# Kernel tuning notes

Measured on AMD Instinct MI355X. Metric: run time of the kernel, lower is better.

The kernel has to match this reference:

```python
import jax, jax.numpy as jnp
import numpy as np

N_PAPER = 100000
N_AUTHOR = 50000
E = 800000
D_IN, D_HID, D_OUT = 128, 128, 64


def seg_max(x, src, dst, num_segments):
    # adj_t.matmul(x, reduce='max'): per-destination max over neighbor features;
    # destinations with no in-edges get 0 (torch_sparse convention).
    m = jax.ops.segment_max(x[src], dst, num_segments=num_segments)
    return jnp.where(jnp.isneginf(m), jnp.zeros((), m.dtype), m)


def setup_inputs() -> dict:
    key = jax.random.key(0)
    ks = jax.random.split(key, 32)
    inp = {}
    inp['x_paper'] = jax.random.normal(ks[0], (N_PAPER, D_IN), jnp.float32)
    inp['emb_author'] = jax.random.normal(ks[1], (N_AUTHOR, D_IN), jnp.float32)
    inp['writes_src'] = jax.random.randint(ks[2], (E,), 0, N_AUTHOR, jnp.int32)
    inp['writes_dst'] = jax.random.randint(ks[3], (E,), 0, N_PAPER, jnp.int32)
    inp['cites_src'] = jax.random.randint(ks[4], (E,), 0, N_PAPER, jnp.int32)
    inp['cites_dst'] = jax.random.randint(ks[5], (E,), 0, N_PAPER, jnp.int32)
    inp['wb_src'] = jax.random.randint(ks[6], (E,), 0, N_PAPER, jnp.int32)
    inp['wb_dst'] = jax.random.randint(ks[7], (E,), 0, N_AUTHOR, jnp.int32)

    def lin_w(k, din, dout):
        s = 1.0 / np.sqrt(din)
        return jax.random.uniform(k, (din, dout), jnp.float32, -s, s)

    # layer 1: D_IN -> D_HID
    inp['w1_rel_writes'] = lin_w(ks[8], D_IN, D_HID)
    inp['w1_rel_cites'] = lin_w(ks[9], D_IN, D_HID)
    inp['w1_rel_wb'] = lin_w(ks[10], D_IN, D_HID)
    inp['w1_root_paper'] = lin_w(ks[11], D_IN, D_HID)
    inp['b1_root_paper'] = jnp.zeros((D_HID,), jnp.float32)
    inp['w1_root_author'] = lin_w(ks[12], D_IN, D_HID)
    inp['b1_root_author'] = jnp.zeros((D_HID,), jnp.float32)
    # layer 2: D_HID -> D_OUT
    inp['w2_rel_writes'] = lin_w(ks[13], D_HID, D_OUT)
    inp['w2_rel_cites'] = lin_w(ks[14], D_HID, D_OUT)
    inp['w2_rel_wb'] = lin_w(ks[15], D_HID, D_OUT)
    inp['w2_root_paper'] = lin_w(ks[16], D_HID, D_OUT)
    inp['b2_root_paper'] = jnp.zeros((D_OUT,), jnp.float32)
    inp['w2_root_author'] = lin_w(ks[17], D_HID, D_OUT)
    inp['b2_root_author'] = jnp.zeros((D_OUT,), jnp.float32)
    return inp


def _conv(xp, xa, edges, w_writes, w_cites, w_wb, w_rp, b_rp, w_ra, b_ra):
    writes_src, writes_dst, cites_src, cites_dst, wb_src, wb_dst = edges
    out_p = xp @ w_rp + b_rp
    out_a = xa @ w_ra + b_ra
    out_p = out_p + seg_max(xa, writes_src, writes_dst, N_PAPER) @ w_writes
    out_p = out_p + seg_max(xp, cites_src, cites_dst, N_PAPER) @ w_cites
    out_a = out_a + seg_max(xp, wb_src, wb_dst, N_AUTHOR) @ w_wb
    return out_p, out_a


def reference(x_paper, emb_author,
              writes_src, writes_dst, cites_src, cites_dst, wb_src, wb_dst,
              w1_rel_writes, w1_rel_cites, w1_rel_wb,
              w1_root_paper, b1_root_paper, w1_root_author, b1_root_author,
              w2_rel_writes, w2_rel_cites, w2_rel_wb,
              w2_root_paper, b2_root_paper, w2_root_author, b2_root_author):
    edges = (writes_src, writes_dst, cites_src, cites_dst, wb_src, wb_dst)
    hp, ha = _conv(x_paper, emb_author, edges,
                   w1_rel_writes, w1_rel_cites, w1_rel_wb,
                   w1_root_paper, b1_root_paper, w1_root_author, b1_root_author)
    hp, ha = jax.nn.relu(hp), jax.nn.relu(ha)  # dropout p=0 -> identity
    return _conv(hp, ha, edges,
                 w2_rel_writes, w2_rel_cites, w2_rel_wb,
                 w2_root_paper, b2_root_paper, w2_root_author, b2_root_author)
```

## Files before the change

kernel.cpp:

```cpp
#include <hip/hip_runtime.h>


#define DI 128
#define NP 100000
#define NA 50000
#define EPB 4096
#define MAXBIN 391

typedef short s8v __attribute__((ext_vector_type(8)));
typedef float f32x4 __attribute__((ext_vector_type(4)));

__device__ __forceinline__ unsigned short bf16_rne(float f) {
  unsigned int fb = __float_as_uint(f);
  fb += 0x7FFFu + ((fb >> 16) & 1u);
  return (unsigned short)(fb >> 16);
}

__global__ __launch_bounds__(256) void cvt2_k(const float* __restrict__ Xp,
                                              unsigned short* __restrict__ Yp, int n4p,
                                              const float* __restrict__ Xa,
                                              unsigned short* __restrict__ Ya, int n4a) {
  int i = blockIdx.x * 256 + threadIdx.x;
  const float* X; unsigned short* Y;
  if (i < n4p) { X = Xp; Y = Yp; }
  else { i -= n4p; if (i >= n4a) return; X = Xa; Y = Ya; }
  float4 f = reinterpret_cast<const float4*>(X)[i];
  ushort4 o;
  o.x = bf16_rne(f.x); o.y = bf16_rne(f.y); o.z = bf16_rne(f.z); o.w = bf16_rne(f.w);
  reinterpret_cast<ushort4*>(Y)[i] = o;
}

struct R3Args {
  const int* src[3]; const int* dst[3];
  int* bh[3]; int* bhs[3];
  unsigned int* tmp[3];
  int* bkt[3]; int* cnt[3]; int* rs[3];
  int E[3]; int N[3]; int nbin[3]; int NB[3];
};

__global__ __launch_bounds__(256) void radix_s1_k(R3Args a) {
  int y = blockIdx.y, blk = blockIdx.x;
  int NB = a.NB[y];
  if (blk >= NB) return;
  __shared__ int hist[MAXBIN];
  int nbin = a.nbin[y];
  for (int i = threadIdx.x; i < nbin; i += 256) hist[i] = 0;
  __syncthreads();
  int e0 = blk * EPB, e1 = min(e0 + EPB, a.E[y]);
  const int* dst = a.dst[y];
  for (int e = e0 + threadIdx.x; e < e1; e += 256)
    atomicAdd(&hist[dst[e] >> 8], 1);
  __syncthreads();
  int* bh = a.bh[y];
  for (int i = threadIdx.x; i < nbin; i += 256) bh[i * NB + blk] = hist[i];
}

__global__ __launch_bounds__(256) void radix_x1_k(R3Args a) {
  int y = blockIdx.y, blk = blockIdx.x;
  int NB = a.NB[y];
  if (blk >= NB) return;
  __shared__ int cur[MAXBIN];
  int nbin = a.nbin[y];
  const int* bhs = a.bhs[y];
  for (int i = threadIdx.x; i < nbin; i += 256) cur[i] = bhs[i * NB + blk];
  __syncthreads();
  int e0 = blk * EPB, e1 = min(e0 + EPB, a.E[y]);
  const int* dst = a.dst[y];
  const int* src = a.src[y];
  unsigned int* tmp = a.tmp[y];
  for (int e = e0 + threadIdx.x; e < e1; e += 256) {
    int d = dst[e];
    int pos = atomicAdd(&cur[d >> 8], 1);
    tmp[pos] = ((unsigned int)(d & 255) << 24) | (unsigned int)src[e];
  }
}

__global__ __launch_bounds__(256) void radix_p2_k(R3Args a) {
  int y = blockIdx.y, bin = blockIdx.x;
  if (bin >= a.nbin[y]) return;
  __shared__ int hist[256], scn[256], cursor[256];
  int t = threadIdx.x;
  hist[t] = 0;
  __syncthreads();
  const int* bhs = a.bhs[y];
  int NB = a.NB[y];
  int base = bhs[bin * NB];
  int end  = (bin + 1 < a.nbin[y]) ? bhs[(bin + 1) * NB] : a.E[y];
  const unsigned int* tmp = a.tmp[y];
  for (int i = base + t; i < end; i += 256)
    atomicAdd(&hist[tmp[i] >> 24], 1);
  __syncthreads();
  int v = hist[t];
  scn[t] = v; __syncthreads();
  int acc = v;
  for (int o = 1; o < 256; o <<= 1) {
    int u = (t >= o) ? scn[t - o] : 0;
    __syncthreads();
    acc += u; scn[t] = acc;
    __syncthreads();
  }
  int ex = acc - v;
  cursor[t] = ex;
  int d = bin * 256 + t;
  if (d < a.N[y]) { a.cnt[y][d] = v; a.rs[y][d] = base + ex; }
  __syncthreads();
  int* bkt = a.bkt[y];
  for (int i = base + t; i < end; i += 256) {
    unsigned int p = tmp[i];
    int pos = atomicAdd(&cursor[p >> 24], 1);
    bkt[base + pos] = (int)(p & 0xFFFFFFu);
  }
}

struct S3Args {
  const int* cnt[3]; int* bsum[3]; int* rs[3];
  int n[3]; int nb[3];
};

__global__ __launch_bounds__(256) void blocksum3_k(S3Args a) {
  int y = blockIdx.y;
  int n = a.n[y];
  if (blockIdx.x * 1024 >= n) return;
  __shared__ int red[256];
  int t = threadIdx.x;
  int base = blockIdx.x * 1024 + t * 4;
  int s = 0;
  #pragma unroll
  for (int i = 0; i < 4; ++i) { int idx = base + i; if (idx < n) s += a.cnt[y][idx]; }
  red[t] = s; __syncthreads();
  #pragma unroll
  for (int o = 128; o > 0; o >>= 1) { if (t < o) red[t] += red[t + o]; __syncthreads(); }
  if (t == 0) a.bsum[y][blockIdx.x] = red[0];
}

__global__ __launch_bounds__(256) void partials3_k(S3Args a) {
  __shared__ int sm[256];
  int y = blockIdx.x;
  int nb = a.nb[y];
  int t = threadIdx.x;
  int v = (t < nb) ? a.bsum[y][t] : 0;
  sm[t] = v; __syncthreads();
  int acc = v;
  for (int o = 1; o < 256; o <<= 1) {
    int u = (t >= o) ? sm[t - o] : 0;
    __syncthreads();
    acc += u; sm[t] = acc;
    __syncthreads();
  }
  if (t < nb) a.bsum[y][t] = acc - v;
}

__global__ __launch_bounds__(256) void scanwrite3_k(S3Args a) {
  int y = blockIdx.y;
  int n = a.n[y];
  if (blockIdx.x * 1024 >= n) return;
  __shared__ int ts[256];
  int t = threadIdx.x;
  int base = blockIdx.x * 1024 + t * 4;
  int v[4]; int s = 0;
  #pragma unroll
  for (int i = 0; i < 4; ++i) { int idx = base + i; v[i] = (idx < n) ? a.cnt[y][idx] : 0; s += v[i]; }
  ts[t] = s; __syncthreads();
  int inc = s;
  for (int o = 1; o < 256; o <<= 1) {
    int u = (t >= o) ? ts[t - o] : 0;
    __syncthreads();
    inc += u; ts[t] = inc;
    __syncthreads();
  }
  int p = a.bsum[y][blockIdx.x] + inc - s;
  #pragma unroll
  for (int i = 0; i < 4; ++i) { int idx = base + i; if (idx < n) { a.rs[y][idx] = p; p += v[i]; } }
}

struct WArgs {
  const float* w[10];
  unsigned short* wf[10];
};
__global__ __launch_bounds__(256) void warrange_k(WArgs args) {
  int widx = blockIdx.y;
  int OUTi = (widx < 5) ? 128 : 64;
  int CF = OUTi / 16;
  int nt = 4 * CF * 64;
  int t = blockIdx.x * 256 + threadIdx.x;
  if (t >= nt) return;
  int lane = t & 63, tmp = t >> 6;
  int cf = tmp % CF, kc = tmp / CF;
  int k0 = kc * 32 + (lane >> 4) * 8;
  int c  = cf * 16 + (lane & 15);
  const float* w = args.w[widx];
  s8v v;
  #pragma unroll
  for (int i = 0; i < 8; ++i) v[i] = (short)bf16_rne(w[(k0 + i) * OUTi + c]);
  *(reinterpret_cast<s8v*>(args.wf[widx]) + t) = v;
}


__device__ __forceinline__ void gather_to_lds(
    unsigned short* __restrict__ ldsT,
    const int* __restrict__ cnt, const int* __restrict__ rs,
    const int* __restrict__ bkt, const unsigned short* __restrict__ X,
    int row0, int N)
{
  const int t = threadIdx.x;
  const int lg = t & 15;
  const int rr = t >> 4;
  #pragma unroll
  for (int pass = 0; pass < 4; ++pass) {
    const int r = pass * 16 + rr;
    const int d = row0 + r;
    uint4 o; o.x = o.y = o.z = o.w = 0u;
    if (d < N) {
      const int deg = cnt[d];
      if (deg > 0) {
        const int* bp = bkt + rs[d];
        float ml[4], mh[4];
        #pragma unroll
        for (int j = 0; j < 4; ++j) { ml[j] = -3.4e38f; mh[j] = -3.4e38f; }
        int s0 = bp[0];
        for (int e = 0; e < deg; e += 2) {
          int s1 = (e + 1 < deg) ? bp[e + 1] : s0;
          int sn = (e + 2 < deg) ? bp[e + 2] : s0;
          uint4 r0 = *reinterpret_cast<const uint4*>(X + (size_t)s0 * DI + lg * 8);
          uint4 r1 = *reinterpret_cast<const uint4*>(X + (size_t)s1 * DI + lg * 8);
          unsigned int w0[4] = {r0.x, r0.y, r0.z, r0.w};
          unsigned int w1[4] = {r1.x, r1.y, r1.z, r1.w};
          #pragma unroll
          for (int j = 0; j < 4; ++j) {
            ml[j] = fmaxf(ml[j], __uint_as_float(w0[j] << 16));
            mh[j] = fmaxf(mh[j], __uint_as_float(w0[j] & 0xFFFF0000u));
            ml[j] = fmaxf(ml[j], __uint_as_float(w1[j] << 16));
            mh[j] = fmaxf(mh[j], __uint_as_float(w1[j] & 0xFFFF0000u));
          }
          s0 = sn;
        }
        o.x = (__float_as_uint(ml[0]) >> 16) | (__float_as_uint(mh[0]) & 0xFFFF0000u);
        o.y = (__float_as_uint(ml[1]) >> 16) | (__float_as_uint(mh[1]) & 0xFFFF0000u);
        o.z = (__float_as_uint(ml[2]) >> 16) | (__float_as_uint(mh[2]) & 0xFFFF0000u);
        o.w = (__float_as_uint(ml[3]) >> 16) | (__float_as_uint(mh[3]) & 0xFFFF0000u);
      }
    }
    const int byte = (r * 256 + lg * 16) ^ ((r & 7) << 4);
    *reinterpret_cast<uint4*>(reinterpret_cast<char*>(ldsT) + byte) = o;
  }
}

template<int CF>
__device__ __forceinline__ void mfma_global(const unsigned short* __restrict__ A,
                                            const unsigned short* __restrict__ W,
                                            f32x4* acc, size_t arow, int lane, int half) {
  const s8v* a = reinterpret_cast<const s8v*>(A + arow * DI + half * 8);
  const s8v* w = reinterpret_cast<const s8v*>(W) + lane;
  #pragma unroll
  for (int kc = 0; kc < 4; ++kc) {
    s8v av = a[kc * 4];
    #pragma unroll
    for (int cf = 0; cf < CF; ++cf)
      acc[cf] = __builtin_amdgcn_mfma_f32_16x16x32_bf16(av, w[(kc * CF + cf) * 64], acc[cf], 0, 0, 0);
  }
}

template<int CF>
__device__ __forceinline__ void mfma_lds(const unsigned short* __restrict__ ldsT,
                                         const unsigned short* __restrict__ W,
                                         f32x4* acc, int wrow, int lane) {
  const int rl = lane & 15, half = lane >> 4;
  const int r = wrow + rl;
  const s8v* w = reinterpret_cast<const s8v*>(W) + lane;
  #pragma unroll
  for (int kc = 0; kc < 4; ++kc) {
    const int byte = (r * 256 + half * 16 + kc * 64) ^ ((r & 7) << 4);
    s8v av = *reinterpret_cast<const s8v*>(reinterpret_cast<const char*>(ldsT) + byte);
    #pragma unroll
    for (int cf = 0; cf < CF; ++cf)
      acc[cf] = __builtin_amdgcn_mfma_f32_16x16x32_bf16(av, w[(kc * CF + cf) * 64], acc[cf], 0, 0, 0);
  }
}

struct FLArgs {
  const unsigned short *root[2], *Wroot[2];
  const unsigned short *feat1[2], *Wrel1[2];
  const unsigned short *feat2,    *Wrel2;
  const int *cnt1[2], *rs1[2], *bkt1[2];
  const int *cnt2,    *rs2,    *bkt2;
  const float* bias[2];
  void* out[2];
  int N[2];
  int blocks0;
};

template<int OUT, bool RELU, bool OUT_BF16>
__global__ __launch_bounds__(256) void fused_layer_k(FLArgs g) {
  constexpr int CF = OUT / 16;
  __shared__ unsigned short lds1[64 * 128];
  __shared__ unsigned short lds2[64 * 128];

  const int p = (blockIdx.x >= (unsigned)g.blocks0) ? 1 : 0;
  const int brow = blockIdx.x - (p ? g.blocks0 : 0);
  const int N = g.N[p];
  const int row0 = brow * 64;
  if (row0 >= N) return;

  gather_to_lds(lds1, g.cnt1[p], g.rs1[p], g.bkt1[p], g.feat1[p], row0, N);
  if (p == 0)
    gather_to_lds(lds2, g.cnt2, g.rs2, g.bkt2, g.feat2, row0, N);
  __syncthreads();

  const int lane = threadIdx.x & 63;
  const int wave = threadIdx.x >> 6;
  const int wrow = wave * 16;
  const int rl = lane & 15, half = lane >> 4;
  const size_t arow = (size_t)(row0 + wrow + rl);

  f32x4 acc[CF];
  #pragma unroll
  for (int i = 0; i < CF; ++i) acc[i] = f32x4{0.f, 0.f, 0.f, 0.f};

  mfma_global<CF>(g.root[p], g.Wroot[p], acc, arow, lane, half);
  mfma_lds<CF>(lds1, g.Wrel1[p], acc, wrow, lane);
  if (p == 0) mfma_lds<CF>(lds2, g.Wrel2, acc, wrow, lane);

  const float* bias = g.bias[p];
  #pragma unroll
  for (int cf = 0; cf < CF; ++cf) {
    float bv = bias[cf * 16 + rl];
    #pragma unroll
    for (int j = 0; j < 4; ++j) {
      int r = row0 + wrow + half * 4 + j;
      if (r >= N) continue;
      float v = acc[cf][j] + bv;
      if (RELU) v = v > 0.f ? v : 0.f;
      size_t idx = (size_t)r * OUT + cf * 16 + rl;
      if (OUT_BF16) ((unsigned short*)g.out[p])[idx] = bf16_rne(v);
      else          ((float*)g.out[p])[idx] = v;
    }
  }
}

extern "C" void kernel_launch(void* const* d_in, const int* in_sizes, int n_in,
                              void* d_out, int out_size, void* d_ws, size_t ws_size,
                              hipStream_t stream) {
  const float* xp = (const float*)d_in[0];
  const float* xa = (const float*)d_in[1];
  const int* wsrc = (const int*)d_in[2];
  const int* wdst = (const int*)d_in[3];
  const int* csrc = (const int*)d_in[4];
  const int* cdst = (const int*)d_in[5];
  const int* bsrc = (const int*)d_in[6];
  const int* bdst = (const int*)d_in[7];
  const int Ew = in_sizes[2], Ec = in_sizes[4], Eb = in_sizes[6];

  const float* w1w  = (const float*)d_in[8];
  const float* w1c  = (const float*)d_in[9];
  const float* w1wb = (const float*)d_in[10];
  const float* w1rp = (const float*)d_in[11];
  const float* b1rp = (const float*)d_in[12];
  const float* w1ra = (const float*)d_in[13];
  const float* b1ra = (const float*)d_in[14];
  const float* w2w  = (const float*)d_in[15];
  const float* w2c  = (const float*)d_in[16];
  const float* w2wb = (const float*)d_in[17];
  const float* w2rp = (const float*)d_in[18];
  const float* b2rp = (const float*)d_in[19];
  const float* w2ra = (const float*)d_in[20];
  const float* b2ra = (const float*)d_in[21];

  char* ws = (char*)d_ws;
  unsigned short* xpb = (unsigned short*)(ws + 0);
  unsigned short* xab = (unsigned short*)(ws + 25600000);
  unsigned short* hp  = (unsigned short*)(ws + 38400000);
  unsigned short* ha  = (unsigned short*)(ws + 64000000);
  int* bkt_w = (int*)(ws + 140800000);
  int* bkt_c = (int*)(ws + 144000000);
  int* bkt_b = (int*)(ws + 147200000);
  int* cnt_w = (int*)(ws + 150400000);
  int* cnt_c = (int*)(ws + 150800000);
  int* cnt_b = (int*)(ws + 151200000);
  int* rs_w  = (int*)(ws + 151400000);
  int* rs_c  = (int*)(ws + 151800000);
  int* rs_b  = (int*)(ws + 152200000);
  int* bsum_w = (int*)(ws + 152400000);
  int* bsum_c = (int*)(ws + 152404096);
  int* bsum_b = (int*)(ws + 152408192);
  unsigned short* wf = (unsigned short*)(ws + 152412288);
  unsigned int* tmp_w = (unsigned int*)(ws + 152660000);
  unsigned int* tmp_c = (unsigned int*)(ws + 155860000);
  unsigned int* tmp_b = (unsigned int*)(ws + 159060000);
  int* bh_w  = (int*)(ws + 76800000);
  int* bh_c  = (int*)(ws + 77110000);
  int* bh_b  = (int*)(ws + 77420000);
  int* bhs_w = (int*)(ws + 77580000);
  int* bhs_c = (int*)(ws + 77890000);
  int* bhs_b = (int*)(ws + 78200000);

  unsigned short* WF[10];
  size_t off = 0;
  for (int i = 0; i < 10; ++i) {
    WF[i] = wf + off;
    off += (i < 5) ? (size_t)128 * 128 : (size_t)128 * 64;
  }
  WArgs wa;
  const float* wsrcs[10] = {w1w, w1c, w1wb, w1rp, w1ra, w2w, w2c, w2wb, w2rp, w2ra};
  for (int i = 0; i < 10; ++i) { wa.w[i] = wsrcs[i]; wa.wf[i] = WF[i]; }

  float* outP = (float*)d_out;
  float* outA = outP + (size_t)NP * 64;

  const int gP = (NP + 63) / 64, gA = (NA + 63) / 64;

  R3Args ra;
  ra.src[0] = wsrc; ra.dst[0] = wdst; ra.E[0] = Ew; ra.N[0] = NP;
  ra.src[1] = csrc; ra.dst[1] = cdst; ra.E[1] = Ec; ra.N[1] = NP;
  ra.src[2] = bsrc; ra.dst[2] = bdst; ra.E[2] = Eb; ra.N[2] = NA;
  ra.bh[0] = bh_w; ra.bh[1] = bh_c; ra.bh[2] = bh_b;
  ra.bhs[0] = bhs_w; ra.bhs[1] = bhs_c; ra.bhs[2] = bhs_b;
  ra.tmp[0] = tmp_w; ra.tmp[1] = tmp_c; ra.tmp[2] = tmp_b;
  ra.bkt[0] = bkt_w; ra.bkt[1] = bkt_c; ra.bkt[2] = bkt_b;
  ra.cnt[0] = cnt_w; ra.cnt[1] = cnt_c; ra.cnt[2] = cnt_b;
  ra.rs[0] = rs_w; ra.rs[1] = rs_c; ra.rs[2] = rs_b;
  int gSX = 0, gSC = 0, maxbin = 0;
  for (int y = 0; y < 3; ++y) {
    ra.nbin[y] = (ra.N[y] + 255) >> 8;
    ra.NB[y] = (ra.E[y] + EPB - 1) / EPB;
    if (ra.NB[y] > gSX) gSX = ra.NB[y];
    if (ra.nbin[y] > maxbin) maxbin = ra.nbin[y];
  }
  S3Args sa;
  sa.bsum[0] = bsum_w; sa.bsum[1] = bsum_c; sa.bsum[2] = bsum_b;
  for (int y = 0; y < 3; ++y) {
    sa.cnt[y] = ra.bh[y]; sa.rs[y] = ra.bhs[y];
    sa.n[y] = ra.nbin[y] * ra.NB[y];
    sa.nb[y] = (sa.n[y] + 1023) / 1024;
    if (sa.nb[y] > gSC) gSC = sa.nb[y];
  }

  FLArgs f1, f2;
  f1.root[0] = xpb; f1.Wroot[0] = WF[3];
  f1.feat1[0] = xab; f1.Wrel1[0] = WF[0];
  f1.cnt1[0] = cnt_w; f1.rs1[0] = rs_w; f1.bkt1[0] = bkt_w;
  f1.feat2 = xpb; f1.Wrel2 = WF[1];
  f1.cnt2 = cnt_c; f1.rs2 = rs_c; f1.bkt2 = bkt_c;
  f1.bias[0] = b1rp; f1.out[0] = hp; f1.N[0] = NP;
  f1.root[1] = xab; f1.Wroot[1] = WF[4];
  f1.feat1[1] = xpb; f1.Wrel1[1] = WF[2];
  f1.cnt1[1] = cnt_b; f1.rs1[1] = rs_b; f1.bkt1[1] = bkt_b;
  f1.bias[1] = b1ra; f1.out[1] = ha; f1.N[1] = NA;
  f1.blocks0 = gP;
  f2.root[0] = hp; f2.Wroot[0] = WF[8];
  f2.feat1[0] = ha; f2.Wrel1[0] = WF[5];
  f2.cnt1[0] = cnt_w; f2.rs1[0] = rs_w; f2.bkt1[0] = bkt_w;
  f2.feat2 = hp; f2.Wrel2 = WF[6];
  f2.cnt2 = cnt_c; f2.rs2 = rs_c; f2.bkt2 = bkt_c;
  f2.bias[0] = b2rp; f2.out[0] = outP; f2.N[0] = NP;
  f2.root[1] = ha; f2.Wroot[1] = WF[9];
  f2.feat1[1] = hp; f2.Wrel1[1] = WF[7];
  f2.cnt1[1] = cnt_b; f2.rs1[1] = rs_b; f2.bkt1[1] = bkt_b;
  f2.bias[1] = b2ra; f2.out[1] = outA; f2.N[1] = NA;
  f2.blocks0 = gP;

  const int n4p = NP * DI / 4, n4a = NA * DI / 4;

  warrange_k<<<dim3(8, 10), 256, 0, stream>>>(wa);
  cvt2_k<<<(n4p + n4a + 255) / 256, 256, 0, stream>>>(xp, xpb, n4p, xa, xab, n4a);

  radix_s1_k<<<dim3(gSX, 3), 256, 0, stream>>>(ra);
  blocksum3_k<<<dim3(gSC, 3), 256, 0, stream>>>(sa);
  partials3_k<<<3, 256, 0, stream>>>(sa);
  scanwrite3_k<<<dim3(gSC, 3), 256, 0, stream>>>(sa);
  radix_x1_k<<<dim3(gSX, 3), 256, 0, stream>>>(ra);
  radix_p2_k<<<dim3(maxbin, 3), 256, 0, stream>>>(ra);

  fused_layer_k<128, true, true><<<gP + gA, 256, 0, stream>>>(f1);
  fused_layer_k<64, false, false><<<gP + gA, 256, 0, stream>>>(f2);
}
```

Baseline: 393.2 us.

## Gather neighbor max directly into MFMA A-operand registers, drop LDS staging

The segment-max gather no longer writes to shared memory followed by a block barrier. Each lane now gathers the exact 32 bf16 features it needs for its MFMA A fragment (row = lane&15, k-slices by half) and packs them straight into registers. This removes the LDS footprint, the __syncthreads and the LDS reads, so waves proceed independently and occupancy can rise. In exchange, each lane now walks one destination's whole edge list with four strided 16-byte loads per neighbor instead of one coalesced load, and it holds more registers (32 float maxima).

Measured after the change: 367.7 us. -6.5%, faster.

```diff
diff --git a/kernel.cpp b/kernel.cpp
--- a/kernel.cpp
+++ b/kernel.cpp
@@ -9,6 +9,7 @@
 
 typedef short s8v __attribute__((ext_vector_type(8)));
 typedef float f32x4 __attribute__((ext_vector_type(4)));
+typedef unsigned int u32x4 __attribute__((ext_vector_type(4)));
 
 __device__ __forceinline__ unsigned short bf16_rne(float f) {
   unsigned int fb = __float_as_uint(f);
@@ -196,55 +197,6 @@
 }
 
 
-__device__ __forceinline__ void gather_to_lds(
-    unsigned short* __restrict__ ldsT,
-    const int* __restrict__ cnt, const int* __restrict__ rs,
-    const int* __restrict__ bkt, const unsigned short* __restrict__ X,
-    int row0, int N)
-{
-  const int t = threadIdx.x;
-  const int lg = t & 15;
-  const int rr = t >> 4;
-  #pragma unroll
-  for (int pass = 0; pass < 4; ++pass) {
-    const int r = pass * 16 + rr;
-    const int d = row0 + r;
-    uint4 o; o.x = o.y = o.z = o.w = 0u;
-    if (d < N) {
-      const int deg = cnt[d];
-      if (deg > 0) {
-        const int* bp = bkt + rs[d];
-        float ml[4], mh[4];
-        #pragma unroll
-        for (int j = 0; j < 4; ++j) { ml[j] = -3.4e38f; mh[j] = -3.4e38f; }
-        int s0 = bp[0];
-        for (int e = 0; e < deg; e += 2) {
-          int s1 = (e + 1 < deg) ? bp[e + 1] : s0;
-          int sn = (e + 2 < deg) ? bp[e + 2] : s0;
-          uint4 r0 = *reinterpret_cast<const uint4*>(X + (size_t)s0 * DI + lg * 8);
-          uint4 r1 = *reinterpret_cast<const uint4*>(X + (size_t)s1 * DI + lg * 8);
-          unsigned int w0[4] = {r0.x, r0.y, r0.z, r0.w};
-          unsigned int w1[4] = {r1.x, r1.y, r1.z, r1.w};
-          #pragma unroll
-          for (int j = 0; j < 4; ++j) {
-            ml[j] = fmaxf(ml[j], __uint_as_float(w0[j] << 16));
-            mh[j] = fmaxf(mh[j], __uint_as_float(w0[j] & 0xFFFF0000u));
-            ml[j] = fmaxf(ml[j], __uint_as_float(w1[j] << 16));
-            mh[j] = fmaxf(mh[j], __uint_as_float(w1[j] & 0xFFFF0000u));
-          }
-          s0 = sn;
-        }
-        o.x = (__float_as_uint(ml[0]) >> 16) | (__float_as_uint(mh[0]) & 0xFFFF0000u);
-        o.y = (__float_as_uint(ml[1]) >> 16) | (__float_as_uint(mh[1]) & 0xFFFF0000u);
-        o.z = (__float_as_uint(ml[2]) >> 16) | (__float_as_uint(mh[2]) & 0xFFFF0000u);
-        o.w = (__float_as_uint(ml[3]) >> 16) | (__float_as_uint(mh[3]) & 0xFFFF0000u);
-      }
-    }
-    const int byte = (r * 256 + lg * 16) ^ ((r & 7) << 4);
-    *reinterpret_cast<uint4*>(reinterpret_cast<char*>(ldsT) + byte) = o;
-  }
-}
-
 template<int CF>
 __device__ __forceinline__ void mfma_global(const unsigned short* __restrict__ A,
                                             const unsigned short* __restrict__ W,
@@ -261,16 +213,57 @@
 }
 
 template<int CF>
-__device__ __forceinline__ void mfma_lds(const unsigned short* __restrict__ ldsT,
-                                         const unsigned short* __restrict__ W,
-                                         f32x4* acc, int wrow, int lane) {
-  const int rl = lane & 15, half = lane >> 4;
-  const int r = wrow + rl;
+__device__ __forceinline__ void gather_mfma(
+    const int* __restrict__ cnt, const int* __restrict__ rs,
+    const int* __restrict__ bkt, const unsigned short* __restrict__ X,
+    const unsigned short* __restrict__ W,
+    f32x4* acc, int d, int N, int half, int lane)
+{
+  float ml[4][4], mh[4][4];
+  int deg = 0, base = 0;
+  if (d < N) { deg = cnt[d]; base = rs[d]; }
+  if (deg > 0) {
+    #pragma unroll
+    for (int kc = 0; kc < 4; ++kc)
+      #pragma unroll
+      for (int j = 0; j < 4; ++j) { ml[kc][j] = -3.4e38f; mh[kc][j] = -3.4e38f; }
+    const int* bp = bkt + base;
+    int s0 = bp[0];
+    for (int e = 0; e < deg; e += 2) {
+      int s1 = (e + 1 < deg) ? bp[e + 1] : s0;
+      int sn = (e + 2 < deg) ? bp[e + 2] : s0;
+      const unsigned short* x0 = X + (size_t)s0 * DI + half * 8;
+      const unsigned short* x1 = X + (size_t)s1 * DI + half * 8;
+      #pragma unroll
+      for (int kc = 0; kc < 4; ++kc) {
+        uint4 r0 = *reinterpret_cast<const uint4*>(x0 + kc * 32);
+        uint4 r1 = *reinterpret_cast<const uint4*>(x1 + kc * 32);
+        unsigned int w0[4] = {r0.x, r0.y, r0.z, r0.w};
+        unsigned int w1[4] = {r1.x, r1.y, r1.z, r1.w};
+        #pragma unroll
+        for (int j = 0; j < 4; ++j) {
+          ml[kc][j] = fmaxf(ml[kc][j], __uint_as_float(w0[j] << 16));
+          mh[kc][j] = fmaxf(mh[kc][j], __uint_as_float(w0[j] & 0xFFFF0000u));
+          ml[kc][j] = fmaxf(ml[kc][j], __uint_as_float(w1[j] << 16));
+          mh[kc][j] = fmaxf(mh[kc][j], __uint_as_float(w1[j] & 0xFFFF0000u));
+        }
+      }
+      s0 = sn;
+    }
+  } else {
+    #pragma unroll
+    for (int kc = 0; kc < 4; ++kc)
+      #pragma unroll
+      for (int j = 0; j < 4; ++j) { ml[kc][j] = 0.f; mh[kc][j] = 0.f; }
+  }
   const s8v* w = reinterpret_cast<const s8v*>(W) + lane;
   #pragma unroll
   for (int kc = 0; kc < 4; ++kc) {
-    const int byte = (r * 256 + half * 16 + kc * 64) ^ ((r & 7) << 4);
-    s8v av = *reinterpret_cast<const s8v*>(reinterpret_cast<const char*>(ldsT) + byte);
+    u32x4 t;
+    #pragma unroll
+    for (int j = 0; j < 4; ++j)
+      t[j] = (__float_as_uint(mh[kc][j]) & 0xFFFF0000u) | (__float_as_uint(ml[kc][j]) >> 16);
+    s8v av = __builtin_bit_cast(s8v, t);
     #pragma unroll
     for (int cf = 0; cf < CF; ++cf)
       acc[cf] = __builtin_amdgcn_mfma_f32_16x16x32_bf16(av, w[(kc * CF + cf) * 64], acc[cf], 0, 0, 0);
@@ -292,33 +285,27 @@
 template<int OUT, bool RELU, bool OUT_BF16>
 __global__ __launch_bounds__(256) void fused_layer_k(FLArgs g) {
   constexpr int CF = OUT / 16;
-  __shared__ unsigned short lds1[64 * 128];
-  __shared__ unsigned short lds2[64 * 128];
-
   const int p = (blockIdx.x >= (unsigned)g.blocks0) ? 1 : 0;
   const int brow = blockIdx.x - (p ? g.blocks0 : 0);
   const int N = g.N[p];
-  const int row0 = brow * 64;
-  if (row0 >= N) return;
-
-  gather_to_lds(lds1, g.cnt1[p], g.rs1[p], g.bkt1[p], g.feat1[p], row0, N);
-  if (p == 0)
-    gather_to_lds(lds2, g.cnt2, g.rs2, g.bkt2, g.feat2, row0, N);
-  __syncthreads();
-
   const int lane = threadIdx.x & 63;
   const int wave = threadIdx.x >> 6;
-  const int wrow = wave * 16;
   const int rl = lane & 15, half = lane >> 4;
-  const size_t arow = (size_t)(row0 + wrow + rl);
+  const int row0 = brow * 64 + wave * 16;
+  if (row0 >= N) return;
+  const int d = row0 + rl;
+  const size_t arow = (size_t)((d < N) ? d : (N - 1));
 
   f32x4 acc[CF];
   #pragma unroll
   for (int i = 0; i < CF; ++i) acc[i] = f32x4{0.f, 0.f, 0.f, 0.f};
 
   mfma_global<CF>(g.root[p], g.Wroot[p], acc, arow, lane, half);
-  mfma_lds<CF>(lds1, g.Wrel1[p], acc, wrow, lane);
-  if (p == 0) mfma_lds<CF>(lds2, g.Wrel2, acc, wrow, lane);
+  gather_mfma<CF>(g.cnt1[p], g.rs1[p], g.bkt1[p], g.feat1[p], g.Wrel1[p],
+                  acc, d, N, half, lane);
+  if (p == 0)
+    gather_mfma<CF>(g.cnt2, g.rs2, g.bkt2, g.feat2, g.Wrel2,
+                    acc, d, N, half, lane);
 
   const float* bias = g.bias[p];
   #pragma unroll
@@ -326,7 +313,7 @@
     float bv = bias[cf * 16 + rl];
     #pragma unroll
     for (int j = 0; j < 4; ++j) {
-      int r = row0 + wrow + half * 4 + j;
+      int r = row0 + half * 4 + j;
       if (r >= N) continue;
       float v = acc[cf][j] + bv;
       if (RELU) v = v > 0.f ? v : 0.f;
```
